# Optimization experiments

Hardware: AMD Instinct MI355X
Metric: run time of the kernel (lower is better)

## Reference

```python
import jax, jax.numpy as jnp
import numpy as np

HID = 4

def setup_inputs() -> dict:
    key = jax.random.key(0)
    ks = jax.random.split(key, 8)
    B, T, F = 4096, 512, 16
    x = jax.random.normal(ks[0], (B, T, F), dtype=jnp.float32)
    # Keras LSTMCell params: kernel [F,4H], recurrent_kernel [H,4H], bias [4H] (gate order i,f,c,o)
    Wk = jax.random.normal(ks[1], (F, 4 * HID), dtype=jnp.float32) * 0.1
    Wr = jax.random.normal(ks[2], (HID, 4 * HID), dtype=jnp.float32) * 0.1
    b = jnp.zeros((4 * HID,), dtype=jnp.float32)
    W1 = jax.random.normal(ks[3], (HID, 64), dtype=jnp.float32) * 0.1
    b1 = jnp.zeros((64,), dtype=jnp.float32)
    W2 = jax.random.normal(ks[4], (64, 5), dtype=jnp.float32) * 0.1
    b2 = jnp.zeros((5,), dtype=jnp.float32)
    return {"x": x, "Wk": Wk, "Wr": Wr, "b": b, "W1": W1, "b1": b1, "W2": W2, "b2": b2}

def _lstm_last_h(x, Wk, Wr, b):
    B = x.shape[0]
    # precompute input projections for all timesteps: [T, B, 4H]
    xg = jnp.einsum('btf,fg->tbg', x, Wk) + b

    def step(carry, xg_t):
        h, c = carry
        gates = xg_t + h @ Wr  # [B, 4H]
        i, f, g, o = jnp.split(gates, 4, axis=-1)
        i = jax.nn.sigmoid(i)
        f = jax.nn.sigmoid(f)
        o = jax.nn.sigmoid(o)
        c = f * c + i * jnp.tanh(g)
        h = o * jnp.tanh(c)
        return (h, c), None

    h0 = jnp.zeros((B, HID), dtype=x.dtype)
    c0 = jnp.zeros((B, HID), dtype=x.dtype)
    (h, _), _ = jax.lax.scan(step, (h0, c0), xg)
    return h  # [B, H] -- RNN returns last output only (return_sequences=False)

def reference(x, Wk, Wr, b, W1, b1, W2, b2):
    h = _lstm_last_h(x, Wk, Wr, b)
    h = jax.nn.relu(h @ W1 + b1)
    return jax.nn.softmax(h @ W2 + b2, axis=-1)  # [B, 5]
```

## Files before the change

kernel.cpp:

```cpp
#include <hip/hip_runtime.h>

#define TLEN 512
#define LOG2E 1.44269504088896340736f

#if __has_builtin(__builtin_amdgcn_exp2f)
#define EXP2F(x) __builtin_amdgcn_exp2f(x)
#else
#define EXP2F(x) __exp2f(x)
#endif
#if __has_builtin(__builtin_amdgcn_rcpf)
#define RCPF(x) __builtin_amdgcn_rcpf(x)
#else
#define RCPF(x) (1.0f / (x))
#endif

#define SWZ(v, xm) __int_as_float(__builtin_amdgcn_ds_swizzle(__float_as_int(v), (((xm) << 10) | 0x1F)))
#define DPPF(v, ctrl) __int_as_float(__builtin_amdgcn_update_dpp(__float_as_int(v), __float_as_int(v), (ctrl), 0xF, 0xF, false))
#define QB(v, k) DPPF(v, 0x55 * (k))
#define XOR3(v)  DPPF(v, 0x1B)
#define XOR7(v)  DPPF(v, 0x141)
#define XOR8(v)  DPPF(v, 0x128)

#define WAITVM(N) { \
    asm volatile("s_waitcnt vmcnt(" #N ")" ::: "memory"); \
    __builtin_amdgcn_sched_barrier(0); }

typedef const __attribute__((address_space(1))) unsigned int gu32;
typedef __attribute__((address_space(3))) unsigned int lu32;

__global__ __launch_bounds__(256)
__attribute__((amdgpu_waves_per_eu(1, 1)))
void lstm_mlp_kernel(
    const float* __restrict__ x,
    const float* __restrict__ Wk,
    const float* __restrict__ Wr,
    const float* __restrict__ bg,
    const float* __restrict__ W1,
    const float* __restrict__ b1,
    const float* __restrict__ W2,
    const float* __restrict__ b2,
    float* __restrict__ out,
    int B)
{
    __shared__ float4 lds[4][4][64];

    const int tidx = threadIdx.x;
    const int w   = tidx >> 6;
    const int L   = tidx & 63;
    const int sl  = (tidx >> 4) & 3;
    const int i16 = tidx & 15;
    const int j   = i16 >> 2;
    const int q   = i16 & 3;
    const int gate = q * 4 + j;
    const int seq = blockIdx.x * 16 + (tidx >> 4);

    const bool is_g = (q == 2);
    const float k1 = is_g ? (-2.0f * LOG2E) : (-LOG2E);
    const float m1c = is_g ? (-4.0f * LOG2E) : 1.0f;
    const float m0c = is_g ? (2.0f * LOG2E) : 0.0f;

    float wk[16];
#pragma unroll
    for (int f = 0; f < 16; ++f) wk[f] = k1 * Wk[f * 16 + gate];
    const float wr0 = k1 * Wr[(j ^ 0) * 16 + gate];
    const float wr1 = k1 * Wr[(j ^ 1) * 16 + gate];
    const float wr2 = k1 * Wr[(j ^ 2) * 16 + gate];
    const float wr3 = k1 * Wr[(j ^ 3) * 16 + gate];
    const float biasS = k1 * bg[gate];

    const int dseq = L & 3;
    const int dtl  = L >> 4;
    const int chnk = (L >> 2) & 3;
    const float* xb = x + ((size_t)(blockIdx.x * 16 + w * 4 + dseq) * TLEN + dtl) * 16 + chnk * 4;

#define DMA(SLOT, T0) \
    __builtin_amdgcn_global_load_lds((gu32*)(const void*)(xb + (size_t)(T0) * 16), \
                                     (lu32*)(void*)(&lds[w][SLOT][0]), 16, 0, 0)

    float cs = 0.0f, h = 0.0f;

#define DOT4S(v, w0_, w1_, w2_, w3_, seed) \
    fmaf((v).x, (w0_), fmaf((v).y, (w1_), fmaf((v).z, (w2_), fmaf((v).w, (w3_), (seed)))))
#define DOTQ(Ra, Rb, Rc, Rd) \
    ((DOT4S((Ra), wk[0], wk[1], wk[2], wk[3], biasS) + \
      DOT4S((Rb), wk[4], wk[5], wk[6], wk[7], 0.0f)) + \
     (DOT4S((Rc), wk[8], wk[9], wk[10], wk[11], 0.0f) + \
      DOT4S((Rd), wk[12], wk[13], wk[14], wk[15], 0.0f)))

#define REFILL(SLOT, XDN) { \
    const float4* lg_ = &lds[w][SLOT][0]; \
    float4 A0=lg_[sl+ 0], A1=lg_[sl+ 4], A2=lg_[sl+ 8], A3=lg_[sl+12]; \
    float4 B0=lg_[sl+16], B1=lg_[sl+20], B2=lg_[sl+24], B3=lg_[sl+28]; \
    float4 C0=lg_[sl+32], C1=lg_[sl+36], C2=lg_[sl+40], C3=lg_[sl+44]; \
    float4 D0=lg_[sl+48], D1=lg_[sl+52], D2=lg_[sl+56], D3=lg_[sl+60]; \
    (XDN).x = DOTQ(A0, A1, A2, A3); \
    (XDN).y = DOTQ(B0, B1, B2, B3); \
    (XDN).z = DOTQ(C0, C1, C2, C3); \
    (XDN).w = DOTQ(D0, D1, D2, D3); }

#define STEP(XD) { \
    float h1_ = XOR7(XOR3(h));    \
    float h2_ = XOR8(h);          \
    float h3_ = XOR8(h1_);        \
    float preA = fmaf(h, wr0, fmaf(h1_, wr1, (XD))); \
    float preB = fmaf(h2_, wr2, h3_ * wr3); \
    float pre = preA + preB; \
    float r_ = RCPF(1.0f + EXP2F(pre)); \
    float av = fmaf(m1c, r_, m0c); \
    float iv = QB(av, 0); \
    float fv = QB(av, 1); \
    float gv = QB(av, 2); \
    float ov = QB(av, 3); \
    cs = fmaf(fv, cs, iv * gv); \
    float th_ = fmaf(2.0f, RCPF(1.0f + EXP2F(cs)), -1.0f); \
    h = ov * th_; }

    WAITVM(0);
    DMA(0, 0);
    DMA(1, 4);
    DMA(2, 8);
    DMA(3, 12);
    WAITVM(3);
    float4 xd;
    REFILL(0, xd);

#pragma clang loop unroll(disable)
    for (int g = 0; g < 127; ++g) {
        WAITVM(2);
        float4 xdn;
        REFILL((g + 1) & 3, xdn);
        STEP(xd.x);
        STEP(xd.y);
        STEP(xd.z);
        STEP(xd.w);
        int t0 = (g + 4) << 2;
        t0 = t0 > (TLEN - 4) ? (TLEN - 4) : t0;
        DMA(g & 3, t0);
        xd = xdn;
    }
    STEP(xd.x);
    STEP(xd.y);
    STEP(xd.z);
    STEP(xd.w);
    WAITVM(0);

    float hA = h;
    float hB = SWZ(h, 4), hC = SWZ(h, 8), hD = SWZ(h, 12);

    float p0 = 0.f, p1 = 0.f, p2 = 0.f, p3 = 0.f, p4 = 0.f;
#pragma unroll
    for (int r = 0; r < 4; ++r) {
        const int u = i16 * 4 + r;
        float acc = b1[u];
        acc = fmaf(hA, W1[(j ^ 0) * 64 + u], acc);
        acc = fmaf(hB, W1[(j ^ 1) * 64 + u], acc);
        acc = fmaf(hC, W1[(j ^ 2) * 64 + u], acc);
        acc = fmaf(hD, W1[(j ^ 3) * 64 + u], acc);
        acc = fmaxf(acc, 0.0f);
        p0 = fmaf(acc, W2[u * 5 + 0], p0);
        p1 = fmaf(acc, W2[u * 5 + 1], p1);
        p2 = fmaf(acc, W2[u * 5 + 2], p2);
        p3 = fmaf(acc, W2[u * 5 + 3], p3);
        p4 = fmaf(acc, W2[u * 5 + 4], p4);
    }
    p0 += SWZ(p0, 1); p1 += SWZ(p1, 1); p2 += SWZ(p2, 1); p3 += SWZ(p3, 1); p4 += SWZ(p4, 1);
    p0 += SWZ(p0, 2); p1 += SWZ(p1, 2); p2 += SWZ(p2, 2); p3 += SWZ(p3, 2); p4 += SWZ(p4, 2);
    p0 += SWZ(p0, 4); p1 += SWZ(p1, 4); p2 += SWZ(p2, 4); p3 += SWZ(p3, 4); p4 += SWZ(p4, 4);
    p0 += SWZ(p0, 8); p1 += SWZ(p1, 8); p2 += SWZ(p2, 8); p3 += SWZ(p3, 8); p4 += SWZ(p4, 8);

    p0 += b2[0]; p1 += b2[1]; p2 += b2[2]; p3 += b2[3]; p4 += b2[4];

    float mx = fmaxf(fmaxf(fmaxf(p0, p1), fmaxf(p2, p3)), p4);
    float e0 = EXP2F((p0 - mx) * LOG2E);
    float e1 = EXP2F((p1 - mx) * LOG2E);
    float e2 = EXP2F((p2 - mx) * LOG2E);
    float e3 = EXP2F((p3 - mx) * LOG2E);
    float e4 = EXP2F((p4 - mx) * LOG2E);
    float s = ((e0 + e1) + (e2 + e3)) + e4;
    float rs = RCPF(s);

    if (i16 == 0) {
        float* op = out + (size_t)seq * 5;
        op[0] = e0 * rs; op[1] = e1 * rs; op[2] = e2 * rs;
        op[3] = e3 * rs; op[4] = e4 * rs;
    }
}

extern "C" void kernel_launch(void* const* d_in, const int* in_sizes, int n_in,
                              void* d_out, int out_size, void* d_ws, size_t ws_size,
                              hipStream_t stream) {
    const float* x  = (const float*)d_in[0];
    const float* Wk = (const float*)d_in[1];
    const float* Wr = (const float*)d_in[2];
    const float* bg = (const float*)d_in[3];
    const float* W1 = (const float*)d_in[4];
    const float* b1 = (const float*)d_in[5];
    const float* W2 = (const float*)d_in[6];
    const float* b2 = (const float*)d_in[7];
    float* out = (float*)d_out;

    const int B = in_sizes[0] / (TLEN * 16);
    dim3 block(256);
    dim3 grid(B / 16);
    lstm_mlp_kernel<<<grid, block, 0, stream>>>(x, Wk, Wr, bg, W1, b1, W2, b2, out, B);
}
```

Before: 82.16 us.

## Deepen LDS prefetch ring to eight slots and interleave loads with recurrence steps

Doubles the LDS staging ring from four to eight slots, so async global-to-LDS copies run further ahead of their use. The per-group refill is split into four per-timestep chunks: each chunk issues its LDS reads, runs one recurrence step, then computes that timestep's input projection for the next group. The aim is to hide memory latency and keep the serial recurrence from waiting on a bulk refill. In exchange it doubles the LDS footprint and adds scheduling barriers that may limit how the compiler overlaps work.

```diff
diff --git a/kernel.cpp b/kernel.cpp
--- a/kernel.cpp
+++ b/kernel.cpp
@@ -42,7 +42,7 @@
     float* __restrict__ out,
     int B)
 {
-    __shared__ float4 lds[4][4][64];
+    __shared__ float4 lds[4][8][64];
 
     const int tidx = threadIdx.x;
     const int w   = tidx >> 6;
@@ -86,17 +86,6 @@
       DOT4S((Rb), wk[4], wk[5], wk[6], wk[7], 0.0f)) + \
      (DOT4S((Rc), wk[8], wk[9], wk[10], wk[11], 0.0f) + \
       DOT4S((Rd), wk[12], wk[13], wk[14], wk[15], 0.0f)))
-
-#define REFILL(SLOT, XDN) { \
-    const float4* lg_ = &lds[w][SLOT][0]; \
-    float4 A0=lg_[sl+ 0], A1=lg_[sl+ 4], A2=lg_[sl+ 8], A3=lg_[sl+12]; \
-    float4 B0=lg_[sl+16], B1=lg_[sl+20], B2=lg_[sl+24], B3=lg_[sl+28]; \
-    float4 C0=lg_[sl+32], C1=lg_[sl+36], C2=lg_[sl+40], C3=lg_[sl+44]; \
-    float4 D0=lg_[sl+48], D1=lg_[sl+52], D2=lg_[sl+56], D3=lg_[sl+60]; \
-    (XDN).x = DOTQ(A0, A1, A2, A3); \
-    (XDN).y = DOTQ(B0, B1, B2, B3); \
-    (XDN).z = DOTQ(C0, C1, C2, C3); \
-    (XDN).w = DOTQ(D0, D1, D2, D3); }
 
 #define STEP(XD) { \
     float h1_ = XOR7(XOR3(h));    \
@@ -115,33 +104,45 @@
     float th_ = fmaf(2.0f, RCPF(1.0f + EXP2F(cs)), -1.0f); \
     h = ov * th_; }
 
+#define BODYK(LG, K, X) { \
+    float4 a_ = (LG)[(K) * 16 + sl]; \
+    float4 b_ = (LG)[(K) * 16 + 4 + sl]; \
+    float4 c_ = (LG)[(K) * 16 + 8 + sl]; \
+    float4 d_ = (LG)[(K) * 16 + 12 + sl]; \
+    __builtin_amdgcn_sched_barrier(0); \
+    STEP(X); \
+    X = DOTQ(a_, b_, c_, d_); }
+
     WAITVM(0);
-    DMA(0, 0);
-    DMA(1, 4);
-    DMA(2, 8);
-    DMA(3, 12);
-    WAITVM(3);
-    float4 xd;
-    REFILL(0, xd);
+    DMA(0, 0);  DMA(1, 4);  DMA(2, 8);  DMA(3, 12);
+    DMA(4, 16); DMA(5, 20); DMA(6, 24); DMA(7, 28);
+    WAITVM(7);
+    float X0, X1, X2, X3;
+    {
+        const float4* lg0 = &lds[w][0][0];
+        float4 a0=lg0[sl+0],  a1=lg0[sl+4],  a2=lg0[sl+8],  a3=lg0[sl+12];
+        float4 b0=lg0[sl+16], b1_=lg0[sl+20], b2_=lg0[sl+24], b3=lg0[sl+28];
+        float4 c0=lg0[sl+32], c1=lg0[sl+36], c2=lg0[sl+40], c3=lg0[sl+44];
+        float4 d0=lg0[sl+48], d1=lg0[sl+52], d2=lg0[sl+56], d3=lg0[sl+60];
+        X0 = DOTQ(a0, a1, a2, a3);
+        X1 = DOTQ(b0, b1_, b2_, b3);
+        X2 = DOTQ(c0, c1, c2, c3);
+        X3 = DOTQ(d0, d1, d2, d3);
+    }
 
 #pragma clang loop unroll(disable)
     for (int g = 0; g < 127; ++g) {
-        WAITVM(2);
-        float4 xdn;
-        REFILL((g + 1) & 3, xdn);
-        STEP(xd.x);
-        STEP(xd.y);
-        STEP(xd.z);
-        STEP(xd.w);
-        int t0 = (g + 4) << 2;
+        WAITVM(6);
+        const float4* lg = &lds[w][(g + 1) & 7][0];
+        BODYK(lg, 0, X0);
+        BODYK(lg, 1, X1);
+        BODYK(lg, 2, X2);
+        BODYK(lg, 3, X3);
+        int t0 = (g + 8) << 2;
         t0 = t0 > (TLEN - 4) ? (TLEN - 4) : t0;
-        DMA(g & 3, t0);
-        xd = xdn;
-    }
-    STEP(xd.x);
-    STEP(xd.y);
-    STEP(xd.z);
-    STEP(xd.w);
+        DMA(g & 7, t0);
+    }
+    STEP(X0); STEP(X1); STEP(X2); STEP(X3);
     WAITVM(0);
 
     float hA = h;
```

New measurement: 93.15 us. 13.4% more time.
